# Kernel optimization log

Hardware: AMD Instinct MI355X
Metric: run time of the kernel (lower is better)

The kernel has to match this reference:

```python
import jax, jax.numpy as jnp
import numpy as np

B, L, H = 32, 2048, 512
EPS = 1e-6


def setup_inputs() -> dict:
    key = jax.random.key(0)
    k1, k2 = jax.random.split(key)
    hidden = jax.random.normal(k1, (B, L, H), dtype=jnp.float32)
    # nn.Linear(H, H): weight [H, H], bias [H]; use kaiming-uniform-like scale
    bound = 1.0 / np.sqrt(H)
    W = jax.random.uniform(k2, (H, H), dtype=jnp.float32, minval=-bound, maxval=bound)
    b = jnp.zeros((H,), dtype=jnp.float32)
    return {"hidden": hidden, "W": W, "b": b}


def reference(hidden, W, b):
    Bn, Ln, Hn = hidden.shape

    def step(M, k):
        # k: [B, H]; key == value == hidden[:, t, :]
        v_pred = jnp.einsum("bij,bj->bi", M, k)               # M @ k
        denom = jnp.sum(k * k, axis=-1, keepdims=True) + EPS   # [B, 1]
        delta_v = k - v_pred / denom                           # v - v_pred/denom (v == k)
        M = M + jnp.einsum("bi,bj->bij", delta_v, k)           # outer-product update
        return M, None

    M0 = jnp.zeros((Bn, Hn, Hn), dtype=hidden.dtype)
    xs = jnp.swapaxes(hidden[:, :-1, :], 0, 1)  # [L-1, B, H]
    M, _ = jax.lax.scan(step, M0, xs)

    query = hidden[:, -1, :]                                   # [B, H]
    context = jnp.einsum("bij,bj->bi", M, query)               # [B, H]
    return context @ W.T + b                                   # read_proj
```

## Files before the change

### kernel.cpp

```cpp
#include <hip/hip_runtime.h>
#include <hip/hip_fp16.h>

#define B_  32
#define L_  2048
#define H_  512
#define CA  64
#define NC  32
#define EPSF 1e-6f

typedef _Float16 f16x8 __attribute__((ext_vector_type(8)));
typedef float f32x16 __attribute__((ext_vector_type(16)));

template <int CTRL>
__device__ __forceinline__ float dpp_shift_add(float x) {
  int t = __builtin_amdgcn_update_dpp(0, __float_as_int(x), CTRL, 0xf, 0xf, true);
  return x + __int_as_float(t);
}
__device__ __forceinline__ float wave_reduce_lane63(float x) {
  x = dpp_shift_add<0x111>(x);
  x = dpp_shift_add<0x112>(x);
  x = dpp_shift_add<0x114>(x);
  x = dpp_shift_add<0x118>(x);
  x = dpp_shift_add<0x142>(x);
  x = dpp_shift_add<0x143>(x);
  return x;
}
__device__ __forceinline__ float rdlane(float v, int l) {
  return __int_as_float(__builtin_amdgcn_readlane(__float_as_int(v), l));
}
__device__ __forceinline__ void load_lds16h(const unsigned short* g, unsigned short* l) {
  __builtin_amdgcn_global_load_lds(
      (const __attribute__((address_space(1))) unsigned int*)(g),
      (__attribute__((address_space(3))) unsigned int*)(l), 16, 0, 0);
}

__global__ __launch_bounds__(256) void
deltarule_gram64(const float* __restrict__ hidden,
                 unsigned short* __restrict__ Kh,
                 float* __restrict__ tmT, float* __restrict__ dvec) {
  const int cb = blockIdx.x, b = blockIdx.y;
  const int tid = threadIdx.x, lane = tid & 63, wv = tid >> 6;
  __shared__ __align__(16) unsigned short Kf[CA * H_];
  __shared__ __align__(16) float G[CA * CA];

  const int c0 = cb * CA;
  const float* src = hidden + ((size_t)b * L_ + c0) * H_;
  unsigned short* kout = Kh + ((size_t)b * L_ + c0) * H_;
  const bool lastc = (cb == NC - 1);

#pragma unroll
  for (int u = 0; u < 16; ++u) {
    const int f8 = u * 256 + tid;
    const int row = f8 >> 6;
    const int colf = (f8 & 63) * 8;
    float4 va = *(const float4*)(src + row * H_ + colf);
    float4 vb = *(const float4*)(src + row * H_ + colf + 4);
    if (lastc && row == CA - 1) {
      va = make_float4(0.f, 0.f, 0.f, 0.f);
      vb = make_float4(0.f, 0.f, 0.f, 0.f);
    }
    __half2 h0 = __floats2half2_rn(va.x, va.y);
    __half2 h1 = __floats2half2_rn(va.z, va.w);
    __half2 h2 = __floats2half2_rn(vb.x, vb.y);
    __half2 h3 = __floats2half2_rn(vb.z, vb.w);
    uint4 pk = make_uint4(*(unsigned int*)&h0, *(unsigned int*)&h1,
                          *(unsigned int*)&h2, *(unsigned int*)&h3);
    *(uint4*)&Kf[((colf >> 3) * CA + row) * 8] = pk;
    *(uint4*)(kout + row * H_ + colf) = pk;
  }
  __syncthreads();

  if (wv < 3) {
    const int ta = (wv == 2) ? 1 : 0;
    const int tb = (wv == 0) ? 0 : 1;
    const int mrow = 32 * ta + (lane & 31);
    const int nrow = 32 * tb + (lane & 31);
    const int khi = lane >> 5;
    f32x16 acc;
#pragma unroll
    for (int r = 0; r < 16; ++r) acc[r] = 0.f;
#pragma unroll
    for (int kk = 0; kk < 32; ++kk) {
      const int k8 = 2 * kk + khi;
      const f16x8 av = *(const f16x8*)&Kf[(k8 * CA + mrow) * 8];
      const f16x8 bv = *(const f16x8*)&Kf[(k8 * CA + nrow) * 8];
      acc = __builtin_amdgcn_mfma_f32_32x32x16_f16(av, bv, acc, 0, 0, 0);
    }
#pragma unroll
    for (int r = 0; r < 16; ++r) {
      const int row32 = (r & 3) + 8 * (r >> 2) + 4 * khi;
      G[(32 * ta + row32) * CA + 32 * tb + (lane & 31)] = acc[r];
    }
  }
  __syncthreads();

  if (tid < CA) dvec[((size_t)b * NC + cb) * CA + tid] = G[tid * CA + tid] + EPSF;
  __syncthreads();

  if (wv == 0) {
    const int j = lane & 31;
    float X[32];
#pragma unroll
    for (int t = 31; t >= 0; --t) {
      float i0 = 0.f, i1 = 0.f;
#pragma unroll
      for (int s = t + 1; s < 32; s += 2) i0 = fmaf(G[t * CA + s], X[s], i0);
#pragma unroll
      for (int s = t + 2; s < 32; s += 2) i1 = fmaf(G[t * CA + s], X[s], i1);
      X[t] = (((j == t) ? 1.f : 0.f) - (i0 + i1)) / (G[t * CA + t] + EPSF);
    }
    if (lane < 32) {
#pragma unroll
      for (int t = 0; t < 32; ++t) G[t * CA + j] = X[t];
    }
  } else if (wv == 1) {
    const int j = lane & 31;
    float X[32];
#pragma unroll
    for (int t = 31; t >= 0; --t) {
      float i0 = 0.f, i1 = 0.f;
#pragma unroll
      for (int s = t + 1; s < 32; s += 2) i0 = fmaf(G[(32 + t) * CA + 32 + s], X[s], i0);
#pragma unroll
      for (int s = t + 2; s < 32; s += 2) i1 = fmaf(G[(32 + t) * CA + 32 + s], X[s], i1);
      X[t] = (((j == t) ? 1.f : 0.f) - (i0 + i1)) / (G[(32 + t) * CA + 32 + t] + EPSF);
    }
    if (lane < 32) {
#pragma unroll
      for (int t = 0; t < 32; ++t) G[(32 + t) * CA + 32 + j] = X[t];
    }
  }
  __syncthreads();

  const int zr = tid >> 3;
  const int zc = (tid & 7) * 4;
  float4 zf = make_float4(0.f, 0.f, 0.f, 0.f);
#pragma unroll
  for (int s = 0; s < 32; ++s) {
    const float u = G[zr * CA + 32 + s];
    const float4 xv = *(const float4*)&G[(32 + s) * CA + 32 + zc];
    zf.x = fmaf(u, xv.x, zf.x); zf.y = fmaf(u, xv.y, zf.y);
    zf.z = fmaf(u, xv.z, zf.z); zf.w = fmaf(u, xv.w, zf.w);
  }
  __syncthreads();
  *(float4*)&G[zr * CA + 32 + zc] = zf;
  __syncthreads();
  float4 yf = make_float4(0.f, 0.f, 0.f, 0.f);
#pragma unroll
  for (int s = 0; s < 32; ++s) {
    const float u = G[zr * CA + s];
    const float4 zv = *(const float4*)&G[s * CA + 32 + zc];
    yf.x = fmaf(u, zv.x, yf.x); yf.y = fmaf(u, zv.y, yf.y);
    yf.z = fmaf(u, zv.z, yf.z); yf.w = fmaf(u, zv.w, yf.w);
  }
  __syncthreads();
  *(float4*)&G[zr * CA + 32 + zc] = make_float4(-yf.x, -yf.y, -yf.z, -yf.w);
  __syncthreads();

  float* tout = tmT + ((size_t)b * NC + cb) * (CA * CA);
#pragma unroll
  for (int v = 0; v < 4; ++v) {
    const int f4 = v * 256 + tid;
    const int s = f4 >> 4;
    const int j4 = (f4 & 15) * 4;
    float4 val;
    if (s >= 32 && j4 < 32) val = make_float4(0.f, 0.f, 0.f, 0.f);
    else                    val = *(const float4*)&G[s * CA + j4];
    *(float4*)(tout + s * CA + j4) = val;
  }
}

__global__ __launch_bounds__(512) void
deltarule_scan64(const float* __restrict__ hidden,
                 const unsigned short* __restrict__ Kh,
                 const float* __restrict__ Wm, const float* __restrict__ bias,
                 const float* __restrict__ tmT, const float* __restrict__ dvec,
                 float* __restrict__ out) {
  const int b = blockIdx.x, tid = threadIdx.x, lane = tid & 63, wv = tid >> 6;
  __shared__ __align__(16) unsigned short KT[2][CA * H_];
  __shared__ float Part[8 * CA];
  __shared__ __align__(16) float Wv[H_];
  __shared__ __align__(16) float Ctx[H_];

  const unsigned short* khb = Kh + (size_t)b * L_ * H_;
  const float* tmb = tmT + (size_t)b * NC * (CA * CA);
  const float* dvb = dvec + (size_t)b * NC * CA;

  float wh = hidden[((size_t)b * L_ + (L_ - 1)) * H_ + tid];
  Wv[tid] = wh;
  float ch = 0.f;

  {
    const unsigned short* s0 = khb + (size_t)(NC - 1) * CA * H_;
#pragma unroll
    for (int u = 0; u < 8; ++u) {
      const int off = (u * 8 + wv) * 512;
      load_lds16h(s0 + off + 8 * lane, &KT[(NC - 1) & 1][off]);
    }
  }
  float4 tA, tB; float dCur;
  {
    const float* tp = tmb + (size_t)(NC - 1) * (CA * CA) + lane * CA + 8 * wv;
    tA = *(const float4*)tp;
    tB = *(const float4*)(tp + 4);
    dCur = dvb[(NC - 1) * CA + lane];
  }
  asm volatile("s_waitcnt vmcnt(0) lgkmcnt(0)\n\ts_barrier" ::: "memory");

  for (int c = NC - 1; c >= 0; --c) {
    const int buf = c & 1;

    float4 nA, nB; float dN = 0.f;
    if (c > 0) {
      const float* tp = tmb + (size_t)(c - 1) * (CA * CA) + lane * CA + 8 * wv;
      nA = *(const float4*)tp;
      nB = *(const float4*)(tp + 4);
      dN = dvb[(c - 1) * CA + lane];
      const unsigned short* s1 = khb + (size_t)(c - 1) * CA * H_;
#pragma unroll
      for (int u = 0; u < 8; ++u) {
        const int off = (u * 8 + wv) * 512;
        load_lds16h(s1 + off + 8 * lane, &KT[buf ^ 1][off]);
      }
    }

    const float4 wa  = *(const float4*)&Wv[8 * lane];
    const float4 wb2 = *(const float4*)&Wv[8 * lane + 4];
    float ysg[8];
#pragma unroll
    for (int i = 0; i < 8; ++i) {
      const uint4 kr = *(const uint4*)&KT[buf][(8 * wv + i) * H_ + 8 * lane];
      const float2 f0 = __half22float2(*(const __half2*)&kr.x);
      const float2 f1 = __half22float2(*(const __half2*)&kr.y);
      const float2 f2 = __half22float2(*(const __half2*)&kr.z);
      const float2 f3 = __half22float2(*(const __half2*)&kr.w);
      float p = f0.x * wa.x;
      p = fmaf(f0.y, wa.y, p); p = fmaf(f1.x, wa.z, p); p = fmaf(f1.y, wa.w, p);
      p = fmaf(f2.x, wb2.x, p); p = fmaf(f2.y, wb2.y, p);
      p = fmaf(f3.x, wb2.z, p); p = fmaf(f3.y, wb2.w, p);
      p = wave_reduce_lane63(p);
      ysg[i] = rdlane(p, 63);
    }

    float sp = ysg[0] * tA.x;
    sp = fmaf(ysg[1], tA.y, sp); sp = fmaf(ysg[2], tA.z, sp);
    sp = fmaf(ysg[3], tA.w, sp); sp = fmaf(ysg[4], tB.x, sp);
    sp = fmaf(ysg[5], tB.y, sp); sp = fmaf(ysg[6], tB.z, sp);
    sp = fmaf(ysg[7], tB.w, sp);
    Part[wv * CA + lane] = sp;
    asm volatile("s_waitcnt lgkmcnt(0)\n\ts_barrier" ::: "memory");

    float sig = Part[lane];
#pragma unroll
    for (int w2 = 1; w2 < 8; ++w2) sig += Part[w2 * CA + lane];
    const float sv = dCur * sig;

    float dw0 = 0.f, dw1 = 0.f, dc0 = 0.f, dc1 = 0.f;
#pragma unroll
    for (int t = 0; t < CA; t += 2) {
      const float kv0 = __half2float(*(const __half*)&KT[buf][t * H_ + tid]);
      const float kv1 = __half2float(*(const __half*)&KT[buf][(t + 1) * H_ + tid]);
      dw0 = fmaf(rdlane(sig, t), kv0, dw0);
      dc0 = fmaf(rdlane(sv, t), kv0, dc0);
      dw1 = fmaf(rdlane(sig, t + 1), kv1, dw1);
      dc1 = fmaf(rdlane(sv, t + 1), kv1, dc1);
    }
    wh -= dw0 + dw1;
    ch += dc0 + dc1;
    Wv[tid] = wh;

    if (c > 0) { dCur = dN; tA = nA; tB = nB; }
    asm volatile("s_waitcnt vmcnt(0) lgkmcnt(0)\n\ts_barrier" ::: "memory");
  }

  Ctx[tid] = ch;
  __syncthreads();
  float acc = bias[tid];
  const float* wr = Wm + (size_t)tid * H_;
#pragma unroll 8
  for (int i = 0; i < H_; i += 4) {
    const float4 w4 = *(const float4*)(wr + i);
    const float4 cv = *(const float4*)&Ctx[i];
    acc = fmaf(w4.x, cv.x, acc); acc = fmaf(w4.y, cv.y, acc);
    acc = fmaf(w4.z, cv.z, acc); acc = fmaf(w4.w, cv.w, acc);
  }
  out[(size_t)b * H_ + tid] = acc;
}

extern "C" void kernel_launch(void* const* d_in, const int* in_sizes, int n_in,
                              void* d_out, int out_size, void* d_ws, size_t ws_size,
                              hipStream_t stream) {
  (void)in_sizes; (void)n_in; (void)out_size; (void)ws_size;
  const float* hidden = (const float*)d_in[0];
  const float* Wm     = (const float*)d_in[1];
  const float* bias   = (const float*)d_in[2];
  float* out = (float*)d_out;

  const size_t szKh = (size_t)B_ * L_ * H_ * sizeof(unsigned short);
  unsigned short* Kh = (unsigned short*)d_ws;
  float* tmT  = (float*)((char*)d_ws + szKh);
  float* dvec = tmT + (size_t)B_ * NC * CA * CA;

  deltarule_gram64<<<dim3(NC, B_), 256, 0, stream>>>(hidden, Kh, tmT, dvec);
  deltarule_scan64<<<B_, 512, 0, stream>>>(hidden, Kh, Wm, bias, tmT, dvec, out);
}
```

Baseline: 344.6 us.

## Widen scan kernel to 1024 threads, splitting W and context updates

The per-batch scan kernel now runs with 1024 threads instead of 512. Half the threads update the running query vector W and the other half accumulate the context, so each thread does one rank-update reduction per chunk instead of two. Each wave now handles 4 key rows of the projection instead of 8, and the final read projection is split across both halves, with the partial sums combined through shared memory. The aim is to shorten the serial per-chunk critical path of a grid with only 32 blocks, at the cost of a 16-way partial-sum reduction, more threads taking part in each barrier, and tighter register limits.

After: 341.0 us. About the same (-1.0%).

```diff
diff --git a/kernel.cpp b/kernel.cpp
--- a/kernel.cpp
+++ b/kernel.cpp
@@ -170,15 +170,15 @@
   }
 }
 
-__global__ __launch_bounds__(512) void
-deltarule_scan64(const float* __restrict__ hidden,
-                 const unsigned short* __restrict__ Kh,
-                 const float* __restrict__ Wm, const float* __restrict__ bias,
-                 const float* __restrict__ tmT, const float* __restrict__ dvec,
-                 float* __restrict__ out) {
+__global__ __launch_bounds__(1024) void
+deltarule_scan64w(const float* __restrict__ hidden,
+                  const unsigned short* __restrict__ Kh,
+                  const float* __restrict__ Wm, const float* __restrict__ bias,
+                  const float* __restrict__ tmT, const float* __restrict__ dvec,
+                  float* __restrict__ out) {
   const int b = blockIdx.x, tid = threadIdx.x, lane = tid & 63, wv = tid >> 6;
   __shared__ __align__(16) unsigned short KT[2][CA * H_];
-  __shared__ float Part[8 * CA];
+  __shared__ __align__(16) float Part[16 * 64];
   __shared__ __align__(16) float Wv[H_];
   __shared__ __align__(16) float Ctx[H_];
 
@@ -186,23 +186,25 @@
   const float* tmb = tmT + (size_t)b * NC * (CA * CA);
   const float* dvb = dvec + (size_t)b * NC * CA;
 
-  float wh = hidden[((size_t)b * L_ + (L_ - 1)) * H_ + tid];
-  Wv[tid] = wh;
-  float ch = 0.f;
+  const int hh = tid & (H_ - 1);
+  const bool wgroup = (tid < H_);
+  float wh = 0.f, ch = 0.f;
+  if (wgroup) {
+    wh = hidden[((size_t)b * L_ + (L_ - 1)) * H_ + tid];
+    Wv[tid] = wh;
+  }
 
   {
     const unsigned short* s0 = khb + (size_t)(NC - 1) * CA * H_;
 #pragma unroll
-    for (int u = 0; u < 8; ++u) {
-      const int off = (u * 8 + wv) * 512;
+    for (int u = 0; u < 4; ++u) {
+      const int off = (u * 16 + wv) * 512;
       load_lds16h(s0 + off + 8 * lane, &KT[(NC - 1) & 1][off]);
     }
   }
-  float4 tA, tB; float dCur;
+  float4 tA; float dCur;
   {
-    const float* tp = tmb + (size_t)(NC - 1) * (CA * CA) + lane * CA + 8 * wv;
-    tA = *(const float4*)tp;
-    tB = *(const float4*)(tp + 4);
+    tA = *(const float4*)(tmb + (size_t)(NC - 1) * (CA * CA) + lane * CA + 4 * wv);
     dCur = dvb[(NC - 1) * CA + lane];
   }
   asm volatile("s_waitcnt vmcnt(0) lgkmcnt(0)\n\ts_barrier" ::: "memory");
@@ -210,81 +212,85 @@
   for (int c = NC - 1; c >= 0; --c) {
     const int buf = c & 1;
 
-    float4 nA, nB; float dN = 0.f;
+    float4 nA; float dN = 0.f;
     if (c > 0) {
-      const float* tp = tmb + (size_t)(c - 1) * (CA * CA) + lane * CA + 8 * wv;
-      nA = *(const float4*)tp;
-      nB = *(const float4*)(tp + 4);
+      nA = *(const float4*)(tmb + (size_t)(c - 1) * (CA * CA) + lane * CA + 4 * wv);
       dN = dvb[(c - 1) * CA + lane];
       const unsigned short* s1 = khb + (size_t)(c - 1) * CA * H_;
 #pragma unroll
-      for (int u = 0; u < 8; ++u) {
-        const int off = (u * 8 + wv) * 512;
+      for (int u = 0; u < 4; ++u) {
+        const int off = (u * 16 + wv) * 512;
         load_lds16h(s1 + off + 8 * lane, &KT[buf ^ 1][off]);
       }
     }
+    asm volatile("" ::: "memory");
 
     const float4 wa  = *(const float4*)&Wv[8 * lane];
     const float4 wb2 = *(const float4*)&Wv[8 * lane + 4];
-    float ysg[8];
-#pragma unroll
-    for (int i = 0; i < 8; ++i) {
-      const uint4 kr = *(const uint4*)&KT[buf][(8 * wv + i) * H_ + 8 * lane];
-      const float2 f0 = __half22float2(*(const __half2*)&kr.x);
-      const float2 f1 = __half22float2(*(const __half2*)&kr.y);
-      const float2 f2 = __half22float2(*(const __half2*)&kr.z);
-      const float2 f3 = __half22float2(*(const __half2*)&kr.w);
-      float p = f0.x * wa.x;
-      p = fmaf(f0.y, wa.y, p); p = fmaf(f1.x, wa.z, p); p = fmaf(f1.y, wa.w, p);
-      p = fmaf(f2.x, wb2.x, p); p = fmaf(f2.y, wb2.y, p);
-      p = fmaf(f3.x, wb2.z, p); p = fmaf(f3.y, wb2.w, p);
+    float ysg[4];
+#pragma unroll
+    for (int i = 0; i < 4; ++i) {
+      const uint4 kr = *(const uint4*)&KT[buf][(4 * wv + i) * H_ + 8 * lane];
+      const __half* kh = (const __half*)&kr;
+      float p =            __half2float(kh[0]) * wa.x;
+      p = fmaf(__half2float(kh[1]), wa.y, p);
+      p = fmaf(__half2float(kh[2]), wa.z, p);
+      p = fmaf(__half2float(kh[3]), wa.w, p);
+      p = fmaf(__half2float(kh[4]), wb2.x, p);
+      p = fmaf(__half2float(kh[5]), wb2.y, p);
+      p = fmaf(__half2float(kh[6]), wb2.z, p);
+      p = fmaf(__half2float(kh[7]), wb2.w, p);
       p = wave_reduce_lane63(p);
       ysg[i] = rdlane(p, 63);
     }
 
     float sp = ysg[0] * tA.x;
-    sp = fmaf(ysg[1], tA.y, sp); sp = fmaf(ysg[2], tA.z, sp);
-    sp = fmaf(ysg[3], tA.w, sp); sp = fmaf(ysg[4], tB.x, sp);
-    sp = fmaf(ysg[5], tB.y, sp); sp = fmaf(ysg[6], tB.z, sp);
-    sp = fmaf(ysg[7], tB.w, sp);
-    Part[wv * CA + lane] = sp;
+    sp = fmaf(ysg[1], tA.y, sp);
+    sp = fmaf(ysg[2], tA.z, sp);
+    sp = fmaf(ysg[3], tA.w, sp);
+    Part[wv * 64 + lane] = sp;
     asm volatile("s_waitcnt lgkmcnt(0)\n\ts_barrier" ::: "memory");
 
     float sig = Part[lane];
 #pragma unroll
-    for (int w2 = 1; w2 < 8; ++w2) sig += Part[w2 * CA + lane];
-    const float sv = dCur * sig;
-
-    float dw0 = 0.f, dw1 = 0.f, dc0 = 0.f, dc1 = 0.f;
-#pragma unroll
-    for (int t = 0; t < CA; t += 2) {
-      const float kv0 = __half2float(*(const __half*)&KT[buf][t * H_ + tid]);
-      const float kv1 = __half2float(*(const __half*)&KT[buf][(t + 1) * H_ + tid]);
-      dw0 = fmaf(rdlane(sig, t), kv0, dw0);
-      dc0 = fmaf(rdlane(sv, t), kv0, dc0);
-      dw1 = fmaf(rdlane(sig, t + 1), kv1, dw1);
-      dc1 = fmaf(rdlane(sv, t + 1), kv1, dc1);
-    }
-    wh -= dw0 + dw1;
-    ch += dc0 + dc1;
-    Wv[tid] = wh;
-
-    if (c > 0) { dCur = dN; tA = nA; tB = nB; }
+    for (int w2 = 1; w2 < 16; ++w2) sig += Part[w2 * 64 + lane];
+    const float src = wgroup ? sig : dCur * sig;
+
+    const unsigned short* kcol = &KT[buf][0] + hh;
+    float a0 = 0.f, a1 = 0.f, a2 = 0.f, a3 = 0.f;
+#pragma unroll
+    for (int t = 0; t < CA; t += 4) {
+      a0 = fmaf(rdlane(src, t + 0), __half2float(*(const __half*)&kcol[(t + 0) * H_]), a0);
+      a1 = fmaf(rdlane(src, t + 1), __half2float(*(const __half*)&kcol[(t + 1) * H_]), a1);
+      a2 = fmaf(rdlane(src, t + 2), __half2float(*(const __half*)&kcol[(t + 2) * H_]), a2);
+      a3 = fmaf(rdlane(src, t + 3), __half2float(*(const __half*)&kcol[(t + 3) * H_]), a3);
+    }
+    const float upd = (a0 + a1) + (a2 + a3);
+    if (wgroup) { wh -= upd; Wv[tid] = wh; }
+    else        { ch += upd; }
+
+    if (c > 0) { dCur = dN; tA = nA; }
     asm volatile("s_waitcnt vmcnt(0) lgkmcnt(0)\n\ts_barrier" ::: "memory");
   }
 
-  Ctx[tid] = ch;
-  __syncthreads();
-  float acc = bias[tid];
-  const float* wr = Wm + (size_t)tid * H_;
+  if (!wgroup) Ctx[hh] = ch;
+  __syncthreads();
+  {
+    const int o = hh, hf = tid >> 9;
+    float acc = 0.f;
+    const float* wr = Wm + (size_t)o * H_ + hf * 256;
+    const float* cx = &Ctx[hf * 256];
 #pragma unroll 8
-  for (int i = 0; i < H_; i += 4) {
-    const float4 w4 = *(const float4*)(wr + i);
-    const float4 cv = *(const float4*)&Ctx[i];
-    acc = fmaf(w4.x, cv.x, acc); acc = fmaf(w4.y, cv.y, acc);
-    acc = fmaf(w4.z, cv.z, acc); acc = fmaf(w4.w, cv.w, acc);
-  }
-  out[(size_t)b * H_ + tid] = acc;
+    for (int i = 0; i < 256; i += 4) {
+      const float4 w4 = *(const float4*)(wr + i);
+      const float4 cv = *(const float4*)(cx + i);
+      acc = fmaf(w4.x, cv.x, acc); acc = fmaf(w4.y, cv.y, acc);
+      acc = fmaf(w4.z, cv.z, acc); acc = fmaf(w4.w, cv.w, acc);
+    }
+    Part[hf * 512 + o] = acc;
+  }
+  __syncthreads();
+  if (wgroup) out[(size_t)b * H_ + tid] = Part[tid] + Part[512 + tid] + bias[tid];
 }
 
 extern "C" void kernel_launch(void* const* d_in, const int* in_sizes, int n_in,
@@ -302,5 +308,5 @@
   float* dvec = tmT + (size_t)B_ * NC * CA * CA;
 
   deltarule_gram64<<<dim3(NC, B_), 256, 0, stream>>>(hidden, Kh, tmT, dvec);
-  deltarule_scan64<<<B_, 512, 0, stream>>>(hidden, Kh, Wm, bias, tmT, dvec, out);
-}
+  deltarule_scan64w<<<B_, 1024, 0, stream>>>(hidden, Kh, Wm, bias, tmT, dvec, out);
+}
```
